# Kernel tuning notes

Hardware: AMD Instinct MI355X
Metric: run time of the kernel (lower is better)

The kernel has to match this reference:

```python
import jax, jax.numpy as jnp
import numpy as np

EPS = 1e-8

def _apply_norms(x):
    # x: [B, C, H, W]; torch .std() is unbiased (ddof=1)
    x_min = x.min(axis=1, keepdims=True)
    x_max = x.max(axis=1, keepdims=True)
    norm_minmax = (x - x_min) / (x_max - x_min + EPS)
    x_mean = x.mean(axis=1, keepdims=True)
    x_std = x.std(axis=1, keepdims=True, ddof=1)
    norm_z = (x - x_mean) / (x_std + EPS)
    b_mean = x.mean(axis=(0, 2, 3), keepdims=True)
    b_std = x.std(axis=(0, 2, 3), keepdims=True, ddof=1)
    norm_bn = (x - b_mean) / (b_std + EPS)
    return [norm_minmax, norm_z, norm_bn]

def _compute_metrics(pred, targ):
    B, C, H, W = pred.shape
    p = pred.reshape(B, C, H * W)
    t = targ.reshape(B, C, H * W)
    # SAM: 1 - cosine similarity over channel dim (torch clamps norms at eps)
    dot = (p * t).sum(axis=1)
    np_ = jnp.maximum(jnp.sqrt((p * p).sum(axis=1)), EPS)
    nt_ = jnp.maximum(jnp.sqrt((t * t).sum(axis=1)), EPS)
    sam = 1.0 - dot / (np_ * nt_)
    # Pearson over channel dim
    p_ctr = p - p.mean(axis=1, keepdims=True)
    t_ctr = t - t.mean(axis=1, keepdims=True)
    cov = (p_ctr * t_ctr).sum(axis=1)
    std_p = jnp.sqrt((p_ctr ** 2).sum(axis=1) + EPS)
    std_t = jnp.sqrt((t_ctr ** 2).sum(axis=1) + EPS)
    pearson = 1.0 - cov / (std_p * std_t)
    # SID: symmetric KL over channel-normalized positive distributions
    p_pos = p - p.min(axis=1, keepdims=True)
    t_pos = t - t.min(axis=1, keepdims=True)
    p_prob = jnp.maximum(p_pos / (p_pos.sum(axis=1, keepdims=True) + EPS), EPS)
    t_prob = jnp.maximum(t_pos / (t_pos.sum(axis=1, keepdims=True) + EPS), EPS)
    log_ratio = jnp.log(p_prob / t_prob)
    d_pt = (p_prob * log_ratio).sum(axis=1)
    d_tp = (t_prob * (-log_ratio)).sum(axis=1)
    sid = d_pt + d_tp
    return sam, pearson, sid  # each [B, H*W]

TOP_K_RATIO = 0.05

def setup_inputs() -> dict:
    key = jax.random.key(0)
    k1, k2 = jax.random.split(key)
    B, C, H, W = 4, 128, 256, 256
    reconstructed = jax.random.normal(k1, (B, C, H, W), dtype=jnp.float32)
    target = jax.random.normal(k2, (B, C, H, W), dtype=jnp.float32)
    loss_weights = jnp.ones((9,), dtype=jnp.float32)
    return {"reconstructed": reconstructed, "target": target, "loss_weights": loss_weights}

def reference(reconstructed, target, loss_weights):
    B, C, H, W = reconstructed.shape
    preds = _apply_norms(reconstructed)
    targs = _apply_norms(target)
    all_losses = []
    for p_norm, t_norm in zip(preds, targs):
        sam, pearson, sid = _compute_metrics(p_norm, t_norm)
        all_losses.extend([sam, pearson, sid])
    stacked = jnp.stack(all_losses, axis=0)  # [9, B, H*W]
    weights = jax.nn.softmax(loss_weights).reshape(9, 1, 1)
    weighted_error_map = (stacked * weights).sum(axis=0)  # [B, H*W]
    err_flat = weighted_error_map.reshape(-1)
    k = max(1, int(err_flat.shape[0] * TOP_K_RATIO))
    top_k_errors, _ = jax.lax.top_k(err_flat, k)
    return jnp.mean(top_k_errors), weighted_error_map.reshape(B, H, W)
```

## Files before the change

kernel.cpp:

```cpp
#include <hip/hip_runtime.h>

#define EPSF 1e-8f
#define CCH 128
#define HWSZ 65536
#define NPIX 262144
#define KTOP 13107
#define LN2F 0.6931471805599453f

#define WS_SUM    0
#define WS_CST    512
#define WS_WGT    1024
#define WS_MINKEY 1040
#define WS_MAXKEY 1041
#define WS_BSTAR  1042
#define WS_CNTAB  1043
#define WS_LO2    1044
#define WS_W2     1045
#define WS_K2     1046
#define WS_SUMAB  1048
#define WS_H1     1056
#define WS_H2C    5152
#define WS_H2S    9248
#define WS_TOTAL  13344

__device__ __forceinline__ unsigned fkey(float f){
  unsigned u = __float_as_uint(f);
  return (u & 0x80000000u) ? ~u : (u | 0x80000000u);
}
__device__ __forceinline__ float funkey(unsigned k){
  unsigned u = (k & 0x80000000u) ? (k & 0x7fffffffu) : ~k;
  return __uint_as_float(u);
}

__global__ __launch_bounds__(256) void initWs(unsigned* __restrict__ wsu){
  int idx = blockIdx.x*256 + threadIdx.x;
  if (idx < WS_TOTAL) wsu[idx] = (idx == WS_MINKEY) ? 0xFFFFFFFFu : 0u;
}

__global__ __launch_bounds__(512) void bnSumKernel(const float* __restrict__ rec,
                                                   const float* __restrict__ tgt,
                                                   float* __restrict__ wsf){
  int blk = blockIdx.x;
  int tensor = blk >> 9;
  int rem = blk & 511;
  int c = rem & 127;
  int b = rem >> 7;
  const float* src = (tensor==0 ? rec : tgt) + ((size_t)(b*CCH + c))*HWSZ;
  const float4* src4 = (const float4*)src;
  float s=0.f, q=0.f;
  #pragma unroll 4
  for (int j=threadIdx.x; j<HWSZ/4; j+=512){
    float4 v = src4[j];
    s += v.x+v.y+v.z+v.w;
    q += v.x*v.x + v.y*v.y + v.z*v.z + v.w*v.w;
  }
  for (int off=1; off<64; off<<=1){ s += __shfl_xor(s,off); q += __shfl_xor(q,off); }
  __shared__ float ls[8], lq[8];
  int wid = threadIdx.x >> 6;
  if ((threadIdx.x & 63)==0){ ls[wid]=s; lq[wid]=q; }
  __syncthreads();
  if (threadIdx.x==0){
    float S=0,Q=0;
    for (int i=0;i<8;i++){ S+=ls[i]; Q+=lq[i]; }
    atomicAdd(&wsf[tensor*256 + c], S);
    atomicAdd(&wsf[tensor*256 + 128 + c], Q);
  }
}

__global__ __launch_bounds__(256) void finalizeKernel(const float* __restrict__ lw,
                                                      float* __restrict__ wsf){
  int tid = threadIdx.x;
  {
    int tensor = tid >> 7;
    int c = tid & 127;
    float S = wsf[tensor*256 + c];
    float Q = wsf[tensor*256 + 128 + c];
    const float N = 262144.f;
    float mean = S / N;
    float var = fmaxf((Q - S*S/N) / (N - 1.f), 0.f);
    float inv = 1.f/(sqrtf(var)+EPSF);
    wsf[WS_CST + c*4 + tensor*2 + 0] = inv;
    wsf[WS_CST + c*4 + tensor*2 + 1] = mean*inv;
  }
  if (tid==0){
    float m = -1e30f;
    for (int i=0;i<9;i++) m = fmaxf(m, lw[i]);
    float e[9], sum=0.f;
    for (int i=0;i<9;i++){ e[i]=expf(lw[i]-m); sum+=e[i]; }
    for (int i=0;i<9;i++) wsf[WS_WGT+i] = e[i]/sum;
  }
}

__global__ __launch_bounds__(256) void mainKernel(const float* __restrict__ rec,
                                                  const float* __restrict__ tgt,
                                                  const float* __restrict__ wsf,
                                                  unsigned* __restrict__ wsu,
                                                  float* __restrict__ errMap){
  __shared__ float4 cst[128];
  __shared__ float wgt[12];
  __shared__ float rmn[4], rmx[4];
  int tid = threadIdx.x;
  if (tid < 128) cst[tid] = ((const float4*)(wsf + WS_CST))[tid];
  if (tid < 9)  wgt[tid] = wsf[WS_WGT + tid];
  __syncthreads();

  int pix = blockIdx.x*256 + tid;
  int b = pix >> 16;
  int hw = pix & (HWSZ-1);
  const float* pP = rec + ((size_t)b*CCH)*HWSZ + hw;
  const float* tP = tgt + ((size_t)b*CCH)*HWSZ + hw;

  float psum=0,psumsq=0,tsum=0,tsumsq=0,ptsum=0;
  float pmin=3.4e38f,pmax=-3.4e38f,tmin=3.4e38f,tmax=-3.4e38f;
  float bS1=0,bS11=0,bS2=0,bS22=0,bS12=0,bMp=3.4e38f,bMt=3.4e38f;

  #pragma unroll 8
  for (int c=0;c<CCH;c++){
    float pv = pP[(size_t)c*HWSZ];
    float tv = tP[(size_t)c*HWSZ];
    float4 k = cst[c];
    psum+=pv; psumsq=fmaf(pv,pv,psumsq);
    tsum+=tv; tsumsq=fmaf(tv,tv,tsumsq);
    ptsum=fmaf(pv,tv,ptsum);
    pmin=fminf(pmin,pv); pmax=fmaxf(pmax,pv);
    tmin=fminf(tmin,tv); tmax=fmaxf(tmax,tv);
    float bp = fmaf(pv, k.x, -k.y);
    float bt = fmaf(tv, k.z, -k.w);
    bS1+=bp; bS11=fmaf(bp,bp,bS11);
    bS2+=bt; bS22=fmaf(bt,bt,bS22);
    bS12=fmaf(bp,bt,bS12);
    bMp=fminf(bMp,bp); bMt=fminf(bMt,bt);
  }

  const float Ci = 1.0f/128.0f;
  float smm_p = 1.f/(pmax-pmin+EPSF);
  float smm_t = 1.f/(tmax-tmin+EPSF);
  float mean_p = psum*Ci, mean_t = tsum*Ci;
  float var_p = fmaxf((psumsq - psum*psum*Ci)*(1.f/127.f), 0.f);
  float var_t = fmaxf((tsumsq - tsum*tsum*Ci)*(1.f/127.f), 0.f);
  float zi_p = 1.f/(sqrtf(var_p)+EPSF);
  float zi_t = 1.f/(sqrtf(var_t)+EPSF);

  auto metrics = [](float S1,float S11,float S2,float S22,float S12,
                    float& sam,float& pear){
    float npn = fmaxf(sqrtf(fmaxf(S11,0.f)), EPSF);
    float ntn = fmaxf(sqrtf(fmaxf(S22,0.f)), EPSF);
    sam = 1.f - S12/(npn*ntn);
    const float ci = 1.0f/128.0f;
    float cov = S12 - S1*S2*ci;
    float vp = fmaxf(S11 - S1*S1*ci, 0.f);
    float vt = fmaxf(S22 - S2*S2*ci, 0.f);
    pear = 1.f - cov/(sqrtf(vp+EPSF)*sqrtf(vt+EPSF));
  };
  auto affine = [&](float ap,float sp,float at,float st,float& sam,float& pear){
    float S1 = (psum - 128.f*ap)*sp;
    float S11 = (psumsq - 2.f*ap*psum + 128.f*ap*ap)*sp*sp;
    float S2 = (tsum - 128.f*at)*st;
    float S22 = (tsumsq - 2.f*at*tsum + 128.f*at*at)*st*st;
    float S12 = (ptsum - at*psum - ap*tsum + 128.f*ap*at)*sp*st;
    metrics(S1,S11,S2,S22,S12,sam,pear);
  };

  float sam_mm,pear_mm,sam_z,pear_z,sam_bn,pear_bn;
  affine(pmin,smm_p,tmin,smm_t,sam_mm,pear_mm);
  affine(mean_p,zi_p,mean_t,zi_t,sam_z,pear_z);
  metrics(bS1,bS11,bS2,bS22,bS12,sam_bn,pear_bn);

  float dp = fmaf(psum - 128.f*pmin, smm_p, EPSF);
  float fp = smm_p/dp;  float Bp = pmin*fp;
  float dt = fmaf(tsum - 128.f*tmin, smm_t, EPSF);
  float ft = smm_t/dt;  float Bt = tmin*ft;
  float fbp = 1.f/((bS1 - 128.f*bMp) + EPSF); float Bbp = bMp*fbp;
  float fbt = 1.f/((bS2 - 128.f*bMt) + EPSF); float Bbt = bMt*fbt;

  float sid_mm=0.f, sid_bn=0.f;
  #pragma unroll 8
  for (int c=0;c<CCH;c++){
    float pv = pP[(size_t)c*HWSZ];
    float tv = tP[(size_t)c*HWSZ];
    float4 k = cst[c];
    float pp = fmaxf(fmaf(pv,fp,-Bp), EPSF);
    float tp = fmaxf(fmaf(tv,ft,-Bt), EPSF);
    sid_mm = fmaf(pp-tp, __log2f(pp)-__log2f(tp), sid_mm);
    float bp = fmaf(pv, k.x, -k.y);
    float bt = fmaf(tv, k.z, -k.w);
    float qp = fmaxf(fmaf(bp,fbp,-Bbp), EPSF);
    float qt = fmaxf(fmaf(bt,fbt,-Bbt), EPSF);
    sid_bn = fmaf(qp-qt, __log2f(qp)-__log2f(qt), sid_bn);
  }
  sid_mm *= LN2F; sid_bn *= LN2F;

  float err = wgt[0]*sam_mm + wgt[1]*pear_mm + (wgt[2]+wgt[5])*sid_mm
            + wgt[3]*sam_z  + wgt[4]*pear_z
            + wgt[6]*sam_bn + wgt[7]*pear_bn + wgt[8]*sid_bn;
  errMap[pix] = err;

  float emin = err, emax = err;
  #pragma unroll
  for (int off=1; off<64; off<<=1){
    emin = fminf(emin, __shfl_xor(emin,off));
    emax = fmaxf(emax, __shfl_xor(emax,off));
  }
  int w = tid>>6;
  if ((tid&63)==0){ rmn[w]=emin; rmx[w]=emax; }
  __syncthreads();
  if (tid==0){
    emin = fminf(fminf(rmn[0],rmn[1]),fminf(rmn[2],rmn[3]));
    emax = fmaxf(fmaxf(rmx[0],rmx[1]),fmaxf(rmx[2],rmx[3]));
    atomicMin(&wsu[WS_MINKEY], fkey(emin));
    atomicMax(&wsu[WS_MAXKEY], fkey(emax));
  }
}

__global__ __launch_bounds__(256) void hist1Kernel(const float* __restrict__ err,
                                                   unsigned* __restrict__ wsu){
  __shared__ unsigned h[4096];
  int tid = threadIdx.x;
  for (int i=tid;i<4096;i+=256) h[i]=0u;
  __syncthreads();
  float lo = funkey(wsu[WS_MINKEY]);
  float hi = funkey(wsu[WS_MAXKEY]);
  float invw = 4096.f / fmaxf(hi-lo, 1e-30f);
  int base = blockIdx.x*2048 + tid;
  for (int j=0;j<8;j++){
    float v = err[base + j*256];
    int idx = (int)fminf(fmaxf((v-lo)*invw, 0.f), 4095.f);
    atomicAdd(&h[idx], 1u);
  }
  __syncthreads();
  for (int i=tid;i<4096;i+=256){ unsigned c=h[i]; if (c) atomicAdd(&wsu[WS_H1+i], c); }
}

__global__ __launch_bounds__(256) void scan1Kernel(float* __restrict__ wsf,
                                                   unsigned* __restrict__ wsu){
  __shared__ unsigned counts[4096];
  __shared__ unsigned s[256];
  int tid = threadIdx.x;
  for (int i=tid;i<4096;i+=256) counts[i]=wsu[WS_H1+i];
  __syncthreads();
  unsigned part=0;
  for (int j=0;j<16;j++) part += counts[tid*16+j];
  s[tid]=part; __syncthreads();
  for (int off=1; off<256; off<<=1){
    unsigned v = (tid+off<256)? s[tid+off] : 0u;
    __syncthreads();
    s[tid] += v;
    __syncthreads();
  }
  float lo = funkey(wsu[WS_MINKEY]);
  float hi = funkey(wsu[WS_MAXKEY]);
  float w1 = fmaxf(hi-lo, 1e-30f) * (1.f/4096.f);
  unsigned cum = (tid<255)? s[tid+1] : 0u;
  for (int j=15;j>=0;j--){
    int bin = tid*16+j;
    unsigned cn = cum + counts[bin];
    if (cum < (unsigned)KTOP && cn >= (unsigned)KTOP){
      wsu[WS_BSTAR] = (unsigned)bin;
      wsu[WS_CNTAB] = cum;
      wsu[WS_K2]    = (unsigned)KTOP - cum;
      wsf[WS_LO2]   = lo + (float)bin*w1;
      wsf[WS_W2]    = w1*(1.f/4096.f);
    }
    cum = cn;
  }
}

__global__ __launch_bounds__(256) void hist2Kernel(const float* __restrict__ err,
                                                   float* __restrict__ wsf,
                                                   unsigned* __restrict__ wsu){
  __shared__ unsigned h2[4096];
  __shared__ float s2[4096];
  __shared__ float ls[4];
  int tid = threadIdx.x;
  for (int i=tid;i<4096;i+=256){ h2[i]=0u; s2[i]=0.f; }
  __syncthreads();
  float lo = funkey(wsu[WS_MINKEY]);
  float hi = funkey(wsu[WS_MAXKEY]);
  float invw = 4096.f / fmaxf(hi-lo, 1e-30f);
  int bstar = (int)wsu[WS_BSTAR];
  float lo2 = wsf[WS_LO2];
  float w2  = wsf[WS_W2];
  float invw2 = 1.f / w2;
  float mySum = 0.f;
  int base = blockIdx.x*2048 + tid;
  for (int j=0;j<8;j++){
    float v = err[base + j*256];
    int idx = (int)fminf(fmaxf((v-lo)*invw, 0.f), 4095.f);
    if (idx > bstar){
      mySum += v;
    } else if (idx == bstar){
      int i2 = (int)fminf(fmaxf((v-lo2)*invw2, 0.f), 4095.f);
      atomicAdd(&h2[i2], 1u);
      atomicAdd(&s2[i2], v);
    }
  }
  for (int off=1; off<64; off<<=1) mySum += __shfl_xor(mySum, off);
  if ((tid&63)==0) ls[tid>>6] = mySum;
  __syncthreads();
  if (tid==0) atomicAdd(&wsf[WS_SUMAB], ls[0]+ls[1]+ls[2]+ls[3]);
  for (int i=tid;i<4096;i+=256){
    unsigned c = h2[i]; if (c) atomicAdd(&wsu[WS_H2C+i], c);
    float sv = s2[i];   if (sv != 0.f) atomicAdd(&wsf[WS_H2S+i], sv);
  }
}

__global__ __launch_bounds__(256) void scan2Kernel(float* __restrict__ wsf,
                                                   unsigned* __restrict__ wsu,
                                                   float* __restrict__ out){
  __shared__ unsigned cnt[4096];
  __shared__ float sm[4096];
  __shared__ unsigned sC[256];
  __shared__ float sS[256];
  int tid = threadIdx.x;
  for (int i=tid;i<4096;i+=256){ cnt[i]=wsu[WS_H2C+i]; sm[i]=wsf[WS_H2S+i]; }
  __syncthreads();
  unsigned pc=0; float ps=0.f;
  for (int j=0;j<16;j++){ pc+=cnt[tid*16+j]; ps+=sm[tid*16+j]; }
  sC[tid]=pc; sS[tid]=ps; __syncthreads();
  for (int off=1; off<256; off<<=1){
    unsigned vc = (tid+off<256)? sC[tid+off] : 0u;
    float vs    = (tid+off<256)? sS[tid+off] : 0.f;
    __syncthreads();
    sC[tid] += vc; sS[tid] += vs;
    __syncthreads();
  }
  unsigned k2 = wsu[WS_K2];
  float lo2 = wsf[WS_LO2], w2 = wsf[WS_W2];
  unsigned cum = (tid<255)? sC[tid+1] : 0u;
  float cums   = (tid<255)? sS[tid+1] : 0.f;
  for (int j=15;j>=0;j--){
    int bin = tid*16+j;
    unsigned cn = cum + cnt[bin];
    float sn = cums + sm[bin];
    if (cum < k2 && cn >= k2){
      float val = lo2 + ((float)bin + 0.5f)*w2;
      float total = wsf[WS_SUMAB] + cums + (float)(k2 - cum)*val;
      out[0] = total / (float)KTOP;
    }
    cum = cn; cums = sn;
  }
}

extern "C" void kernel_launch(void* const* d_in, const int* in_sizes, int n_in,
                              void* d_out, int out_size, void* d_ws, size_t ws_size,
                              hipStream_t stream){
  const float* rec = (const float*)d_in[0];
  const float* tgt = (const float*)d_in[1];
  const float* lw  = (const float*)d_in[2];
  float* out = (float*)d_out;
  float* wsf = (float*)d_ws;
  unsigned* wsu = (unsigned*)d_ws;

  hipLaunchKernelGGL(initWs, dim3((WS_TOTAL+255)/256), dim3(256), 0, stream, wsu);
  hipLaunchKernelGGL(bnSumKernel, dim3(1024), dim3(512), 0, stream, rec, tgt, wsf);
  hipLaunchKernelGGL(finalizeKernel, dim3(1), dim3(256), 0, stream, lw, wsf);
  hipLaunchKernelGGL(mainKernel, dim3(NPIX/256), dim3(256), 0, stream, rec, tgt, wsf, wsu, out+1);
  hipLaunchKernelGGL(hist1Kernel, dim3(128), dim3(256), 0, stream, out+1, wsu);
  hipLaunchKernelGGL(scan1Kernel, dim3(1), dim3(256), 0, stream, wsf, wsu);
  hipLaunchKernelGGL(hist2Kernel, dim3(128), dim3(256), 0, stream, out+1, wsf, wsu);
  hipLaunchKernelGGL(scan2Kernel, dim3(1), dim3(256), 0, stream, wsf, wsu, out);
}
```

Before: 198.7 us.

## Process two pixels per thread with float2 loads in main kernel

```diff
diff --git a/kernel.cpp b/kernel.cpp
--- a/kernel.cpp
+++ b/kernel.cpp
@@ -30,6 +30,60 @@
 __device__ __forceinline__ float funkey(unsigned k){
   unsigned u = (k & 0x80000000u) ? (k & 0x7fffffffu) : ~k;
   return __uint_as_float(u);
+}
+
+struct Stats {
+  float psum,psumsq,tsum,tsumsq,ptsum,pmin,pmax,tmin,tmax;
+  float bS1,bS11,bS2,bS22,bS12,bMp,bMt;
+};
+struct Consts { float errBase,fp,Bp,ft,Bt,fbp,Bbp,fbt,Bbt,sidW,bnW; };
+
+__device__ Consts pixEpilogue(const Stats& s, const float* wgt){
+  const float Ci = 1.0f/128.0f;
+  float smm_p = 1.f/(s.pmax-s.pmin+EPSF);
+  float smm_t = 1.f/(s.tmax-s.tmin+EPSF);
+  float mean_p = s.psum*Ci, mean_t = s.tsum*Ci;
+  float var_p = fmaxf((s.psumsq - s.psum*s.psum*Ci)*(1.f/127.f), 0.f);
+  float var_t = fmaxf((s.tsumsq - s.tsum*s.tsum*Ci)*(1.f/127.f), 0.f);
+  float zi_p = 1.f/(sqrtf(var_p)+EPSF);
+  float zi_t = 1.f/(sqrtf(var_t)+EPSF);
+
+  auto metrics = [&](float S1,float S11,float S2,float S22,float S12,
+                     float& sam,float& pear){
+    float npn = fmaxf(sqrtf(fmaxf(S11,0.f)), EPSF);
+    float ntn = fmaxf(sqrtf(fmaxf(S22,0.f)), EPSF);
+    sam = 1.f - S12/(npn*ntn);
+    float cov = S12 - S1*S2*Ci;
+    float vp = fmaxf(S11 - S1*S1*Ci, 0.f);
+    float vt = fmaxf(S22 - S2*S2*Ci, 0.f);
+    pear = 1.f - cov/(sqrtf(vp+EPSF)*sqrtf(vt+EPSF));
+  };
+  auto affine = [&](float ap,float sp,float at,float st,float& sam,float& pear){
+    float S1 = (s.psum - 128.f*ap)*sp;
+    float S11 = (s.psumsq - 2.f*ap*s.psum + 128.f*ap*ap)*sp*sp;
+    float S2 = (s.tsum - 128.f*at)*st;
+    float S22 = (s.tsumsq - 2.f*at*s.tsum + 128.f*at*at)*st*st;
+    float S12 = (s.ptsum - at*s.psum - ap*s.tsum + 128.f*ap*at)*sp*st;
+    metrics(S1,S11,S2,S22,S12,sam,pear);
+  };
+
+  float sam_mm,pear_mm,sam_z,pear_z,sam_bn,pear_bn;
+  affine(s.pmin,smm_p,s.tmin,smm_t,sam_mm,pear_mm);
+  affine(mean_p,zi_p,mean_t,zi_t,sam_z,pear_z);
+  metrics(s.bS1,s.bS11,s.bS2,s.bS22,s.bS12,sam_bn,pear_bn);
+
+  Consts c;
+  c.errBase = wgt[0]*sam_mm + wgt[1]*pear_mm + wgt[3]*sam_z + wgt[4]*pear_z
+            + wgt[6]*sam_bn + wgt[7]*pear_bn;
+  float dp = fmaf(s.psum - 128.f*s.pmin, smm_p, EPSF);
+  c.fp = smm_p/dp;  c.Bp = s.pmin*c.fp;
+  float dt = fmaf(s.tsum - 128.f*s.tmin, smm_t, EPSF);
+  c.ft = smm_t/dt;  c.Bt = s.tmin*c.ft;
+  c.fbp = 1.f/((s.bS1 - 128.f*s.bMp) + EPSF); c.Bbp = s.bMp*c.fbp;
+  c.fbt = 1.f/((s.bS2 - 128.f*s.bMt) + EPSF); c.Bbt = s.bMt*c.fbt;
+  c.sidW = (wgt[2]+wgt[5])*LN2F;
+  c.bnW  = wgt[8]*LN2F;
+  return c;
 }
 
 __global__ __launch_bounds__(256) void initWs(unsigned* __restrict__ wsu){
@@ -91,111 +145,105 @@
   }
 }
 
-__global__ __launch_bounds__(256) void mainKernel(const float* __restrict__ rec,
-                                                  const float* __restrict__ tgt,
-                                                  const float* __restrict__ wsf,
-                                                  unsigned* __restrict__ wsu,
-                                                  float* __restrict__ errMap){
+__global__ __launch_bounds__(256, 4) void mainKernel(const float* __restrict__ rec,
+                                                     const float* __restrict__ tgt,
+                                                     const float* __restrict__ wsf,
+                                                     unsigned* __restrict__ wsu,
+                                                     float* __restrict__ errMap){
   __shared__ float4 cst[128];
-  __shared__ float wgt[12];
+  __shared__ float wgtS[12];
   __shared__ float rmn[4], rmx[4];
   int tid = threadIdx.x;
   if (tid < 128) cst[tid] = ((const float4*)(wsf + WS_CST))[tid];
-  if (tid < 9)  wgt[tid] = wsf[WS_WGT + tid];
-  __syncthreads();
-
-  int pix = blockIdx.x*256 + tid;
-  int b = pix >> 16;
-  int hw = pix & (HWSZ-1);
-  const float* pP = rec + ((size_t)b*CCH)*HWSZ + hw;
-  const float* tP = tgt + ((size_t)b*CCH)*HWSZ + hw;
-
-  float psum=0,psumsq=0,tsum=0,tsumsq=0,ptsum=0;
-  float pmin=3.4e38f,pmax=-3.4e38f,tmin=3.4e38f,tmax=-3.4e38f;
-  float bS1=0,bS11=0,bS2=0,bS22=0,bS12=0,bMp=3.4e38f,bMt=3.4e38f;
-
-  #pragma unroll 8
-  for (int c=0;c<CCH;c++){
-    float pv = pP[(size_t)c*HWSZ];
-    float tv = tP[(size_t)c*HWSZ];
-    float4 k = cst[c];
-    psum+=pv; psumsq=fmaf(pv,pv,psumsq);
-    tsum+=tv; tsumsq=fmaf(tv,tv,tsumsq);
-    ptsum=fmaf(pv,tv,ptsum);
-    pmin=fminf(pmin,pv); pmax=fmaxf(pmax,pv);
-    tmin=fminf(tmin,tv); tmax=fmaxf(tmax,tv);
-    float bp = fmaf(pv, k.x, -k.y);
-    float bt = fmaf(tv, k.z, -k.w);
-    bS1+=bp; bS11=fmaf(bp,bp,bS11);
-    bS2+=bt; bS22=fmaf(bt,bt,bS22);
-    bS12=fmaf(bp,bt,bS12);
-    bMp=fminf(bMp,bp); bMt=fminf(bMt,bt);
-  }
-
-  const float Ci = 1.0f/128.0f;
-  float smm_p = 1.f/(pmax-pmin+EPSF);
-  float smm_t = 1.f/(tmax-tmin+EPSF);
-  float mean_p = psum*Ci, mean_t = tsum*Ci;
-  float var_p = fmaxf((psumsq - psum*psum*Ci)*(1.f/127.f), 0.f);
-  float var_t = fmaxf((tsumsq - tsum*tsum*Ci)*(1.f/127.f), 0.f);
-  float zi_p = 1.f/(sqrtf(var_p)+EPSF);
-  float zi_t = 1.f/(sqrtf(var_t)+EPSF);
-
-  auto metrics = [](float S1,float S11,float S2,float S22,float S12,
-                    float& sam,float& pear){
-    float npn = fmaxf(sqrtf(fmaxf(S11,0.f)), EPSF);
-    float ntn = fmaxf(sqrtf(fmaxf(S22,0.f)), EPSF);
-    sam = 1.f - S12/(npn*ntn);
-    const float ci = 1.0f/128.0f;
-    float cov = S12 - S1*S2*ci;
-    float vp = fmaxf(S11 - S1*S1*ci, 0.f);
-    float vt = fmaxf(S22 - S2*S2*ci, 0.f);
-    pear = 1.f - cov/(sqrtf(vp+EPSF)*sqrtf(vt+EPSF));
-  };
-  auto affine = [&](float ap,float sp,float at,float st,float& sam,float& pear){
-    float S1 = (psum - 128.f*ap)*sp;
-    float S11 = (psumsq - 2.f*ap*psum + 128.f*ap*ap)*sp*sp;
-    float S2 = (tsum - 128.f*at)*st;
-    float S22 = (tsumsq - 2.f*at*tsum + 128.f*at*at)*st*st;
-    float S12 = (ptsum - at*psum - ap*tsum + 128.f*ap*at)*sp*st;
-    metrics(S1,S11,S2,S22,S12,sam,pear);
-  };
-
-  float sam_mm,pear_mm,sam_z,pear_z,sam_bn,pear_bn;
-  affine(pmin,smm_p,tmin,smm_t,sam_mm,pear_mm);
-  affine(mean_p,zi_p,mean_t,zi_t,sam_z,pear_z);
-  metrics(bS1,bS11,bS2,bS22,bS12,sam_bn,pear_bn);
-
-  float dp = fmaf(psum - 128.f*pmin, smm_p, EPSF);
-  float fp = smm_p/dp;  float Bp = pmin*fp;
-  float dt = fmaf(tsum - 128.f*tmin, smm_t, EPSF);
-  float ft = smm_t/dt;  float Bt = tmin*ft;
-  float fbp = 1.f/((bS1 - 128.f*bMp) + EPSF); float Bbp = bMp*fbp;
-  float fbt = 1.f/((bS2 - 128.f*bMt) + EPSF); float Bbt = bMt*fbt;
-
-  float sid_mm=0.f, sid_bn=0.f;
-  #pragma unroll 8
-  for (int c=0;c<CCH;c++){
-    float pv = pP[(size_t)c*HWSZ];
-    float tv = tP[(size_t)c*HWSZ];
-    float4 k = cst[c];
-    float pp = fmaxf(fmaf(pv,fp,-Bp), EPSF);
-    float tp = fmaxf(fmaf(tv,ft,-Bt), EPSF);
-    sid_mm = fmaf(pp-tp, __log2f(pp)-__log2f(tp), sid_mm);
-    float bp = fmaf(pv, k.x, -k.y);
-    float bt = fmaf(tv, k.z, -k.w);
-    float qp = fmaxf(fmaf(bp,fbp,-Bbp), EPSF);
-    float qt = fmaxf(fmaf(bt,fbt,-Bbt), EPSF);
-    sid_bn = fmaf(qp-qt, __log2f(qp)-__log2f(qt), sid_bn);
-  }
-  sid_mm *= LN2F; sid_bn *= LN2F;
-
-  float err = wgt[0]*sam_mm + wgt[1]*pear_mm + (wgt[2]+wgt[5])*sid_mm
-            + wgt[3]*sam_z  + wgt[4]*pear_z
-            + wgt[6]*sam_bn + wgt[7]*pear_bn + wgt[8]*sid_bn;
-  errMap[pix] = err;
-
-  float emin = err, emax = err;
+  if (tid < 9)  wgtS[tid] = wsf[WS_WGT + tid];
+  __syncthreads();
+
+  int pix0 = blockIdx.x*512 + tid*2;
+  int b = pix0 >> 16;
+  unsigned hwb = (unsigned)(pix0 & (HWSZ-1)) * 4u;
+  const char* pB = (const char*)(rec + ((size_t)b*CCH)*HWSZ) + hwb;
+  const char* tB = (const char*)(tgt + ((size_t)b*CCH)*HWSZ) + hwb;
+
+  float2 psum={0,0},psumsq={0,0},tsum={0,0},tsumsq={0,0},ptsum={0,0};
+  float2 pmin={3.4e38f,3.4e38f},pmax={-3.4e38f,-3.4e38f};
+  float2 tmin={3.4e38f,3.4e38f},tmax={-3.4e38f,-3.4e38f};
+  float2 bS1={0,0},bS11={0,0},bS2={0,0},bS22={0,0},bS12={0,0};
+  float2 bMp={3.4e38f,3.4e38f},bMt={3.4e38f,3.4e38f};
+
+  for (int cb=0; cb<CCH; cb+=8){
+    float2 P[8], T[8];
+    #pragma unroll
+    for (int j=0;j<8;j++){
+      P[j] = *(const float2*)(pB + ((unsigned)(cb+j)<<18));
+      T[j] = *(const float2*)(tB + ((unsigned)(cb+j)<<18));
+    }
+    #pragma unroll
+    for (int j=0;j<8;j++){
+      float4 k = cst[cb+j];
+      float2 pv=P[j], tv=T[j];
+      psum.x+=pv.x; psum.y+=pv.y;
+      psumsq.x=fmaf(pv.x,pv.x,psumsq.x); psumsq.y=fmaf(pv.y,pv.y,psumsq.y);
+      tsum.x+=tv.x; tsum.y+=tv.y;
+      tsumsq.x=fmaf(tv.x,tv.x,tsumsq.x); tsumsq.y=fmaf(tv.y,tv.y,tsumsq.y);
+      ptsum.x=fmaf(pv.x,tv.x,ptsum.x); ptsum.y=fmaf(pv.y,tv.y,ptsum.y);
+      pmin.x=fminf(pmin.x,pv.x); pmin.y=fminf(pmin.y,pv.y);
+      pmax.x=fmaxf(pmax.x,pv.x); pmax.y=fmaxf(pmax.y,pv.y);
+      tmin.x=fminf(tmin.x,tv.x); tmin.y=fminf(tmin.y,tv.y);
+      tmax.x=fmaxf(tmax.x,tv.x); tmax.y=fmaxf(tmax.y,tv.y);
+      float bpx = fmaf(pv.x,k.x,-k.y), bpy = fmaf(pv.y,k.x,-k.y);
+      float btx = fmaf(tv.x,k.z,-k.w), bty = fmaf(tv.y,k.z,-k.w);
+      bS1.x+=bpx; bS1.y+=bpy;
+      bS11.x=fmaf(bpx,bpx,bS11.x); bS11.y=fmaf(bpy,bpy,bS11.y);
+      bS2.x+=btx; bS2.y+=bty;
+      bS22.x=fmaf(btx,btx,bS22.x); bS22.y=fmaf(bty,bty,bS22.y);
+      bS12.x=fmaf(bpx,btx,bS12.x); bS12.y=fmaf(bpy,bty,bS12.y);
+      bMp.x=fminf(bMp.x,bpx); bMp.y=fminf(bMp.y,bpy);
+      bMt.x=fminf(bMt.x,btx); bMt.y=fminf(bMt.y,bty);
+    }
+  }
+
+  Stats sx = {psum.x,psumsq.x,tsum.x,tsumsq.x,ptsum.x,pmin.x,pmax.x,tmin.x,tmax.x,
+              bS1.x,bS11.x,bS2.x,bS22.x,bS12.x,bMp.x,bMt.x};
+  Stats sy = {psum.y,psumsq.y,tsum.y,tsumsq.y,ptsum.y,pmin.y,pmax.y,tmin.y,tmax.y,
+              bS1.y,bS11.y,bS2.y,bS22.y,bS12.y,bMp.y,bMt.y};
+  Consts cx = pixEpilogue(sx, wgtS);
+  Consts cy = pixEpilogue(sy, wgtS);
+
+  float2 sid_mm={0,0}, sid_bn={0,0};
+  for (int cb=0; cb<CCH; cb+=8){
+    float2 P[8], T[8];
+    #pragma unroll
+    for (int j=0;j<8;j++){
+      P[j] = *(const float2*)(pB + ((unsigned)(cb+j)<<18));
+      T[j] = *(const float2*)(tB + ((unsigned)(cb+j)<<18));
+    }
+    #pragma unroll
+    for (int j=0;j<8;j++){
+      float4 k = cst[cb+j];
+      float2 pv=P[j], tv=T[j];
+      float ppx = fmaxf(fmaf(pv.x,cx.fp,-cx.Bp), EPSF);
+      float tpx = fmaxf(fmaf(tv.x,cx.ft,-cx.Bt), EPSF);
+      sid_mm.x = fmaf(ppx-tpx, __log2f(ppx)-__log2f(tpx), sid_mm.x);
+      float ppy = fmaxf(fmaf(pv.y,cy.fp,-cy.Bp), EPSF);
+      float tpy = fmaxf(fmaf(tv.y,cy.ft,-cy.Bt), EPSF);
+      sid_mm.y = fmaf(ppy-tpy, __log2f(ppy)-__log2f(tpy), sid_mm.y);
+      float bpx = fmaf(pv.x,k.x,-k.y), bpy = fmaf(pv.y,k.x,-k.y);
+      float btx = fmaf(tv.x,k.z,-k.w), bty = fmaf(tv.y,k.z,-k.w);
+      float qpx = fmaxf(fmaf(bpx,cx.fbp,-cx.Bbp), EPSF);
+      float qtx = fmaxf(fmaf(btx,cx.fbt,-cx.Bbt), EPSF);
+      sid_bn.x = fmaf(qpx-qtx, __log2f(qpx)-__log2f(qtx), sid_bn.x);
+      float qpy = fmaf(bpy,cy.fbp,-cy.Bbp);  qpy = fmaxf(qpy, EPSF);
+      float qty = fmaf(bty,cy.fbt,-cy.Bbt);  qty = fmaxf(qty, EPSF);
+      sid_bn.y = fmaf(qpy-qty, __log2f(qpy)-__log2f(qty), sid_bn.y);
+    }
+  }
+
+  float errx = cx.errBase + cx.sidW*sid_mm.x + cx.bnW*sid_bn.x;
+  float erry = cy.errBase + cy.sidW*sid_mm.y + cy.bnW*sid_bn.y;
+  errMap[pix0]   = errx;
+  errMap[pix0+1] = erry;
+
+  float emin = fminf(errx,erry), emax = fmaxf(errx,erry);
   #pragma unroll
   for (int off=1; off<64; off<<=1){
     emin = fminf(emin, __shfl_xor(emin,off));
@@ -354,7 +402,7 @@
   hipLaunchKernelGGL(initWs, dim3((WS_TOTAL+255)/256), dim3(256), 0, stream, wsu);
   hipLaunchKernelGGL(bnSumKernel, dim3(1024), dim3(512), 0, stream, rec, tgt, wsf);
   hipLaunchKernelGGL(finalizeKernel, dim3(1), dim3(256), 0, stream, lw, wsf);
-  hipLaunchKernelGGL(mainKernel, dim3(NPIX/256), dim3(256), 0, stream, rec, tgt, wsf, wsu, out+1);
+  hipLaunchKernelGGL(mainKernel, dim3(NPIX/512), dim3(256), 0, stream, rec, tgt, wsf, wsu, out+1);
   hipLaunchKernelGGL(hist1Kernel, dim3(128), dim3(256), 0, stream, out+1, wsu);
   hipLaunchKernelGGL(scan1Kernel, dim3(1), dim3(256), 0, stream, wsf, wsu);
   hipLaunchKernelGGL(hist2Kernel, dim3(128), dim3(256), 0, stream, out+1, wsf, wsu);
```

Result: faster. 162.2 us (-18.4%).
